# Kernel optimization log

Measured on AMD Instinct MI355X. Metric: run time of the kernel, lower is better.

The kernel has to match this reference:

```python
import jax, jax.numpy as jnp
import numpy as np

B, N, D = 8, 1024, 1024

def setup_inputs() -> dict:
    key = jax.random.key(0)
    k1, k2, k3, k4, k5 = jax.random.split(key, 5)
    x = jax.random.normal(k1, (B, N, D), dtype=jnp.float32)
    y = jax.random.normal(k2, (B, N, D), dtype=jnp.float32)
    adj = jax.random.uniform(k3, (B, N, N), dtype=jnp.float32)
    adj_sumrow = jnp.sum(adj, axis=-1, keepdims=True)  # [B, N, 1], row-sum normalizer
    W = jax.random.normal(k4, (D, D), dtype=jnp.float32) * (1.0 / np.sqrt(D))
    b = jax.random.normal(k5, (D,), dtype=jnp.float32) * 0.02
    return {"x": x, "y": y, "adj": adj, "adj_sumrow": adj_sumrow, "W": W, "b": b}

def reference(x, y, adj, adj_sumrow, W, b):
    # GraphConvolutionCustom: project neighbor features, aggregate via dense adj,
    # normalize by row-sum, add bias and residual input x; then ReLU.
    # Dropout is identity in eval mode (training=False).
    support = jnp.einsum('bnd,de->bne', y, W)          # [B, N, D]
    agg = jnp.matmul(adj, support) / adj_sumrow        # [B, N, D]
    out = jax.nn.relu(agg + b + x)
    return out
```

## Files before the change

### kernel.cpp

```cpp
#include <hip/hip_runtime.h>
#include <hip/hip_bf16.h>
#include <stdint.h>


typedef float  f32x4  __attribute__((ext_vector_type(4)));
typedef __bf16 bf16x8 __attribute__((ext_vector_type(8)));

__device__ __forceinline__ unsigned short f2bf(float f) {
  union { float f; unsigned int u; } c; c.f = f;
  unsigned int u = c.u;
  u += 0x7FFFu + ((u >> 16) & 1u);
  return (unsigned short)(u >> 16);
}

__device__ __forceinline__ void async_cp16(const void* g, void* l) {
  __builtin_amdgcn_global_load_lds(
      (const __attribute__((address_space(1))) unsigned int*)g,
      (__attribute__((address_space(3))) unsigned int*)l, 16, 0, 0);
}

__device__ __forceinline__ void bar() { asm volatile("s_barrier" ::: "memory"); }


__global__ __launch_bounds__(256) void k_prep(
    const float4* __restrict__ y4, const float4* __restrict__ a4,
    ushort4* __restrict__ yb, ushort4* __restrict__ ab,
    const float* __restrict__ W, unsigned short* __restrict__ Wt)
{
  __shared__ float t[64][65];
  const int bid = blockIdx.x;
  if (bid < 16384) {
    const int i = bid * 256 + threadIdx.x;
    const bool isY = i < 2097152;
    const float4 v = isY ? y4[i] : a4[i - 2097152];
    ushort4 p;
    p.x = f2bf(v.x); p.y = f2bf(v.y); p.z = f2bf(v.z); p.w = f2bf(v.w);
    if (isY) yb[i] = p; else ab[i - 2097152] = p;
  } else {
    const int id = bid - 16384;
    const int n0 = (id & 15) * 64, k0 = (id >> 4) * 64;
    const int tx = threadIdx.x & 63, ty = threadIdx.x >> 6;
#pragma unroll
    for (int r = ty; r < 64; r += 4)
      t[r][tx] = W[(size_t)(k0 + r) * 1024 + n0 + tx];
    __syncthreads();
#pragma unroll
    for (int r = ty; r < 64; r += 4)
      Wt[(size_t)(n0 + r) * 1024 + k0 + tx] = f2bf(t[tx][r]);
  }
}


__device__ __forceinline__ void stage64(
    const unsigned short* __restrict__ A,  int sA,
    const unsigned short* __restrict__ Bt, int sB,
    int m0, int n0, int k0,
    unsigned short* la, unsigned short* lb,
    int wave, int rg, int colo)
{
#pragma unroll
  for (int s = 0; s < 4; ++s) {
    const int t = wave * 4 + s;
    async_cp16(A  + (size_t)(m0 + t * 8 + rg) * sA + k0 + colo, la + t * 512);
    async_cp16(Bt + (size_t)(n0 + t * 8 + rg) * sB + k0 + colo, lb + t * 512);
  }
}

__device__ __forceinline__ void compute64(
    const unsigned short* la, const unsigned short* lb,
    f32x4 acc[4][4], int wm, int wn, int quad, int l16)
{
#pragma unroll
  for (int h = 0; h < 2; ++h) {
    bf16x8 af[4], bfr[4];
#pragma unroll
    for (int i = 0; i < 4; ++i) {
      const int r = wm + i * 16 + l16;
      af[i] = *(const bf16x8*)(la + r * 64 + ((h * 4 + quad + r) & 7) * 8);
    }
#pragma unroll
    for (int j = 0; j < 4; ++j) {
      const int r = wn + j * 16 + l16;
      bfr[j] = *(const bf16x8*)(lb + r * 64 + ((h * 4 + quad + r) & 7) * 8);
    }
#pragma unroll
    for (int i = 0; i < 4; ++i)
#pragma unroll
      for (int j = 0; j < 4; ++j)
        acc[i][j] = __builtin_amdgcn_mfma_f32_16x16x32_bf16(af[i], bfr[j], acc[i][j], 0, 0, 0);
  }
}

__device__ __forceinline__ void gemm_dbuf(
    const unsigned short* __restrict__ A,  int sA,
    const unsigned short* __restrict__ Bt, int sB,
    int m0, int n0, f32x4 acc[4][4], unsigned short* lsm, int tid)
{
  const int lane = tid & 63, wave = tid >> 6;
  const int wm = (wave >> 1) * 64, wn = (wave & 1) * 64;
  const int quad = lane >> 4, l16 = lane & 15;
  const int rg = lane >> 3;
  const int colo = (((lane & 7) - rg) & 7) * 8;
  unsigned short* la0 = lsm;
  unsigned short* lb0 = lsm + 8192;
  unsigned short* la1 = lsm + 16384;
  unsigned short* lb1 = lsm + 24576;

  stage64(A, sA, Bt, sB, m0, n0, 0, la0, lb0, wave, rg, colo);
#pragma unroll 1
  for (int k0 = 0; k0 < 1024; k0 += 128) {
    stage64(A, sA, Bt, sB, m0, n0, k0 + 64, la1, lb1, wave, rg, colo);
    asm volatile("s_waitcnt vmcnt(8)" ::: "memory");
    bar();
    compute64(la0, lb0, acc, wm, wn, quad, l16);
    bar();
    if (k0 + 128 < 1024) {
      stage64(A, sA, Bt, sB, m0, n0, k0 + 128, la0, lb0, wave, rg, colo);
      asm volatile("s_waitcnt vmcnt(8)" ::: "memory");
    } else {
      asm volatile("s_waitcnt vmcnt(0)" ::: "memory");
    }
    bar();
    compute64(la1, lb1, acc, wm, wn, quad, l16);
    bar();
  }
}

__device__ __forceinline__ void zero_acc(f32x4 acc[4][4]) {
#pragma unroll
  for (int i = 0; i < 4; ++i)
#pragma unroll
    for (int j = 0; j < 4; ++j)
#pragma unroll
      for (int r = 0; r < 4; ++r) acc[i][j][r] = 0.0f;
}


__global__ __launch_bounds__(256) void k_gemm1(
    const unsigned short* __restrict__ Wt,
    const unsigned short* __restrict__ Ybf,
    unsigned short* __restrict__ Sup2)
{
  __shared__ __align__(16) unsigned short lsm[4 * 8192];
  const int tid = threadIdx.x;
  const int n0 = blockIdx.x * 128, m0 = blockIdx.y * 128;

  f32x4 acc[4][4];
  zero_acc(acc);
  gemm_dbuf(Wt, 1024, Ybf, 1024, m0, n0, acc, lsm, tid);

  const int lane = tid & 63, wave = tid >> 6;
  const int wm = (wave >> 1) * 64, wn = (wave & 1) * 64;
  const int quad = lane >> 4, l16 = lane & 15;
#pragma unroll
  for (int i = 0; i < 4; ++i) {
    const int mb = m0 + wm + i * 16 + quad * 4;
#pragma unroll
    for (int r = 0; r < 4; ++r) {
      unsigned short* row = Sup2 + ((size_t)(mb + r) << 13);
#pragma unroll
      for (int j = 0; j < 4; ++j)
        row[n0 + wn + j * 16 + l16] = f2bf(acc[i][j][r]);
    }
  }
}


__global__ __launch_bounds__(256) void k_gemm2(
    const unsigned short* __restrict__ AdjBf,
    const unsigned short* __restrict__ Sup2,
    const float* __restrict__ x,
    const float* __restrict__ sumrow,
    const float* __restrict__ bias,
    float* __restrict__ out)
{
  __shared__ __align__(16) unsigned short lsm[4 * 8192];
  const int tid = threadIdx.x;
  const int n0 = blockIdx.x * 128, m0 = blockIdx.y * 128, b = blockIdx.z;

  f32x4 acc[4][4];
  zero_acc(acc);
  gemm_dbuf(AdjBf + ((size_t)b << 20), 1024,
            Sup2 + ((size_t)b << 10), 8192,
            m0, n0, acc, lsm, tid);

  const float* xb = x   + ((size_t)b << 20);
  float*       ob = out + ((size_t)b << 20);
  const float* sr = sumrow + ((size_t)b << 10);
  const int lane = tid & 63, wave = tid >> 6;
  const int wm = (wave >> 1) * 64, wn = (wave & 1) * 64;
  const int quad = lane >> 4, l16 = lane & 15;

  float bv[4];
#pragma unroll
  for (int j = 0; j < 4; ++j) bv[j] = bias[n0 + wn + j * 16 + l16];

#pragma unroll
  for (int i = 0; i < 4; ++i) {
    const int mb = m0 + wm + i * 16 + quad * 4;
#pragma unroll
    for (int r = 0; r < 4; ++r) {
      const int m = mb + r;
      const float inv = 1.0f / sr[m];
#pragma unroll
      for (int j = 0; j < 4; ++j) {
        const int n = n0 + wn + j * 16 + l16;
        const size_t idx = (((size_t)m) << 10) + n;
        float v = acc[i][j][r] * inv + bv[j] + xb[idx];
        ob[idx] = fmaxf(v, 0.0f);
      }
    }
  }
}


extern "C" void kernel_launch(void* const* d_in, const int* in_sizes, int n_in,
                              void* d_out, int out_size, void* d_ws, size_t ws_size,
                              hipStream_t stream) {
  const float* x      = (const float*)d_in[0];
  const float* y      = (const float*)d_in[1];
  const float* adj    = (const float*)d_in[2];
  const float* sumrow = (const float*)d_in[3];
  const float* W      = (const float*)d_in[4];
  const float* bias   = (const float*)d_in[5];
  float* out = (float*)d_out;

  char* ws = (char*)d_ws;
  unsigned short* ybf   = (unsigned short*)(ws);
  unsigned short* adjbf = (unsigned short*)(ws + ((size_t)16 << 20));
  unsigned short* wt    = (unsigned short*)(ws + ((size_t)32 << 20));
  unsigned short* sup2  = (unsigned short*)(ws + ((size_t)34 << 20));

  k_prep<<<dim3(16640), dim3(256), 0, stream>>>(
      (const float4*)y, (const float4*)adj, (ushort4*)ybf, (ushort4*)adjbf, W, wt);
  k_gemm1<<<dim3(64, 8), dim3(256), 0, stream>>>(wt, ybf, sup2);
  k_gemm2<<<dim3(8, 8, 8), dim3(256), 0, stream>>>(adjbf, sup2, x, sumrow, bias, out);
}
```

Baseline: 196.7 us.

## Shrink GEMM tiles to 128x64 with K-step 32 for higher occupancy

Both GEMM kernels move from 128x128 output tiles with a 64-wide K stage to 128x64 tiles with a 32-wide K stage. The LDS swizzle changes to fit the 4-chunk rows, launch bounds request 4 blocks per SM, and the grids double. The aim is to fill more CUs, since the old grids had only 512 blocks, and to hide latency through occupancy. The cost is lower arithmetic intensity per tile, more global and LDS traffic, and twice as many barriers per K.

```diff
diff --git a/kernel.cpp b/kernel.cpp
--- a/kernel.cpp
+++ b/kernel.cpp
@@ -20,6 +20,8 @@
 }
 
 __device__ __forceinline__ void bar() { asm volatile("s_barrier" ::: "memory"); }
+
+__device__ __forceinline__ int swz(int c, int r) { return (c + r + (r >> 1)) & 3; }
 
 
 __global__ __launch_bounds__(256) void k_prep(
@@ -51,106 +53,111 @@
 }
 
 
-__device__ __forceinline__ void stage64(
+__device__ __forceinline__ void stage32(
     const unsigned short* __restrict__ A,  int sA,
     const unsigned short* __restrict__ Bt, int sB,
     int m0, int n0, int k0,
     unsigned short* la, unsigned short* lb,
-    int wave, int rg, int colo)
-{
-#pragma unroll
-  for (int s = 0; s < 4; ++s) {
-    const int t = wave * 4 + s;
-    async_cp16(A  + (size_t)(m0 + t * 8 + rg) * sA + k0 + colo, la + t * 512);
-    async_cp16(Bt + (size_t)(n0 + t * 8 + rg) * sB + k0 + colo, lb + t * 512);
-  }
-}
-
-__device__ __forceinline__ void compute64(
+    int wave, int lane)
+{
+  const int p = lane & 3;
+#pragma unroll
+  for (int s = 0; s < 2; ++s) {
+    const int gid = wave * 128 + s * 64 + lane;
+    const int r = gid >> 2;
+    const int c = (p - r - (r >> 1)) & 3;
+    async_cp16(A + (size_t)(m0 + r) * sA + k0 + c * 8,
+               la + (wave * 128 + s * 64) * 8);
+  }
+  {
+    const int gid = wave * 64 + lane;
+    const int r = gid >> 2;
+    const int c = (p - r - (r >> 1)) & 3;
+    async_cp16(Bt + (size_t)(n0 + r) * sB + k0 + c * 8,
+               lb + (wave * 64) * 8);
+  }
+}
+
+__device__ __forceinline__ void compute32(
     const unsigned short* la, const unsigned short* lb,
-    f32x4 acc[4][4], int wm, int wn, int quad, int l16)
-{
-#pragma unroll
-  for (int h = 0; h < 2; ++h) {
-    bf16x8 af[4], bfr[4];
-#pragma unroll
-    for (int i = 0; i < 4; ++i) {
-      const int r = wm + i * 16 + l16;
-      af[i] = *(const bf16x8*)(la + r * 64 + ((h * 4 + quad + r) & 7) * 8);
-    }
-#pragma unroll
-    for (int j = 0; j < 4; ++j) {
-      const int r = wn + j * 16 + l16;
-      bfr[j] = *(const bf16x8*)(lb + r * 64 + ((h * 4 + quad + r) & 7) * 8);
-    }
-#pragma unroll
-    for (int i = 0; i < 4; ++i)
-#pragma unroll
-      for (int j = 0; j < 4; ++j)
-        acc[i][j] = __builtin_amdgcn_mfma_f32_16x16x32_bf16(af[i], bfr[j], acc[i][j], 0, 0, 0);
-  }
-}
-
-__device__ __forceinline__ void gemm_dbuf(
+    f32x4 acc[4][2], int wm, int wn, int quad, int l16)
+{
+  bf16x8 af[4], bfr[2];
+#pragma unroll
+  for (int i = 0; i < 4; ++i) {
+    const int r = wm + i * 16 + l16;
+    af[i] = *(const bf16x8*)(la + r * 32 + swz(quad, r) * 8);
+  }
+#pragma unroll
+  for (int j = 0; j < 2; ++j) {
+    const int r = wn + j * 16 + l16;
+    bfr[j] = *(const bf16x8*)(lb + r * 32 + swz(quad, r) * 8);
+  }
+#pragma unroll
+  for (int i = 0; i < 4; ++i)
+#pragma unroll
+    for (int j = 0; j < 2; ++j)
+      acc[i][j] = __builtin_amdgcn_mfma_f32_16x16x32_bf16(af[i], bfr[j], acc[i][j], 0, 0, 0);
+}
+
+__device__ __forceinline__ void gemm_dbuf32(
     const unsigned short* __restrict__ A,  int sA,
     const unsigned short* __restrict__ Bt, int sB,
-    int m0, int n0, f32x4 acc[4][4], unsigned short* lsm, int tid)
+    int m0, int n0, f32x4 acc[4][2], unsigned short* lsm, int tid)
 {
   const int lane = tid & 63, wave = tid >> 6;
-  const int wm = (wave >> 1) * 64, wn = (wave & 1) * 64;
+  const int wm = (wave >> 1) * 64, wn = (wave & 1) * 32;
   const int quad = lane >> 4, l16 = lane & 15;
-  const int rg = lane >> 3;
-  const int colo = (((lane & 7) - rg) & 7) * 8;
   unsigned short* la0 = lsm;
-  unsigned short* lb0 = lsm + 8192;
-  unsigned short* la1 = lsm + 16384;
-  unsigned short* lb1 = lsm + 24576;
-
-  stage64(A, sA, Bt, sB, m0, n0, 0, la0, lb0, wave, rg, colo);
+  unsigned short* lb0 = lsm + 4096;
+  unsigned short* la1 = lsm + 6144;
+  unsigned short* lb1 = lsm + 10240;
+
+  stage32(A, sA, Bt, sB, m0, n0, 0, la0, lb0, wave, lane);
 #pragma unroll 1
-  for (int k0 = 0; k0 < 1024; k0 += 128) {
-    stage64(A, sA, Bt, sB, m0, n0, k0 + 64, la1, lb1, wave, rg, colo);
-    asm volatile("s_waitcnt vmcnt(8)" ::: "memory");
-    bar();
-    compute64(la0, lb0, acc, wm, wn, quad, l16);
-    bar();
-    if (k0 + 128 < 1024) {
-      stage64(A, sA, Bt, sB, m0, n0, k0 + 128, la0, lb0, wave, rg, colo);
-      asm volatile("s_waitcnt vmcnt(8)" ::: "memory");
+  for (int k0 = 0; k0 < 1024; k0 += 64) {
+    stage32(A, sA, Bt, sB, m0, n0, k0 + 32, la1, lb1, wave, lane);
+    asm volatile("s_waitcnt vmcnt(3)" ::: "memory");
+    bar();
+    compute32(la0, lb0, acc, wm, wn, quad, l16);
+    bar();
+    if (k0 + 64 < 1024) {
+      stage32(A, sA, Bt, sB, m0, n0, k0 + 64, la0, lb0, wave, lane);
+      asm volatile("s_waitcnt vmcnt(3)" ::: "memory");
     } else {
       asm volatile("s_waitcnt vmcnt(0)" ::: "memory");
     }
     bar();
-    compute64(la1, lb1, acc, wm, wn, quad, l16);
-    bar();
-  }
-}
-
-__device__ __forceinline__ void zero_acc(f32x4 acc[4][4]) {
+    compute32(la1, lb1, acc, wm, wn, quad, l16);
+    bar();
+  }
+}
+
+__device__ __forceinline__ void zero_acc(f32x4 acc[4][2]) {
 #pragma unroll
   for (int i = 0; i < 4; ++i)
 #pragma unroll
-    for (int j = 0; j < 4; ++j)
+    for (int j = 0; j < 2; ++j)
 #pragma unroll
       for (int r = 0; r < 4; ++r) acc[i][j][r] = 0.0f;
 }
 
 
-__global__ __launch_bounds__(256) void k_gemm1(
+__global__ __launch_bounds__(256, 4) void k_gemm1(
     const unsigned short* __restrict__ Wt,
     const unsigned short* __restrict__ Ybf,
     unsigned short* __restrict__ Sup2)
 {
-  __shared__ __align__(16) unsigned short lsm[4 * 8192];
+  __shared__ __align__(16) unsigned short lsm[12288];
   const int tid = threadIdx.x;
-  const int n0 = blockIdx.x * 128, m0 = blockIdx.y * 128;
-
-  f32x4 acc[4][4];
+  const int n0 = blockIdx.x * 64, m0 = blockIdx.y * 128;
+
+  f32x4 acc[4][2];
   zero_acc(acc);
-  gemm_dbuf(Wt, 1024, Ybf, 1024, m0, n0, acc, lsm, tid);
+  gemm_dbuf32(Wt, 1024, Ybf, 1024, m0, n0, acc, lsm, tid);
 
   const int lane = tid & 63, wave = tid >> 6;
-  const int wm = (wave >> 1) * 64, wn = (wave & 1) * 64;
+  const int wm = (wave >> 1) * 64, wn = (wave & 1) * 32;
   const int quad = lane >> 4, l16 = lane & 15;
 #pragma unroll
   for (int i = 0; i < 4; ++i) {
@@ -159,14 +166,14 @@
     for (int r = 0; r < 4; ++r) {
       unsigned short* row = Sup2 + ((size_t)(mb + r) << 13);
 #pragma unroll
-      for (int j = 0; j < 4; ++j)
+      for (int j = 0; j < 2; ++j)
         row[n0 + wn + j * 16 + l16] = f2bf(acc[i][j][r]);
     }
   }
 }
 
 
-__global__ __launch_bounds__(256) void k_gemm2(
+__global__ __launch_bounds__(256, 4) void k_gemm2(
     const unsigned short* __restrict__ AdjBf,
     const unsigned short* __restrict__ Sup2,
     const float* __restrict__ x,
@@ -174,26 +181,26 @@
     const float* __restrict__ bias,
     float* __restrict__ out)
 {
-  __shared__ __align__(16) unsigned short lsm[4 * 8192];
+  __shared__ __align__(16) unsigned short lsm[12288];
   const int tid = threadIdx.x;
-  const int n0 = blockIdx.x * 128, m0 = blockIdx.y * 128, b = blockIdx.z;
-
-  f32x4 acc[4][4];
+  const int n0 = blockIdx.x * 64, m0 = blockIdx.y * 128, b = blockIdx.z;
+
+  f32x4 acc[4][2];
   zero_acc(acc);
-  gemm_dbuf(AdjBf + ((size_t)b << 20), 1024,
-            Sup2 + ((size_t)b << 10), 8192,
-            m0, n0, acc, lsm, tid);
+  gemm_dbuf32(AdjBf + ((size_t)b << 20), 1024,
+              Sup2 + ((size_t)b << 10), 8192,
+              m0, n0, acc, lsm, tid);
 
   const float* xb = x   + ((size_t)b << 20);
   float*       ob = out + ((size_t)b << 20);
   const float* sr = sumrow + ((size_t)b << 10);
   const int lane = tid & 63, wave = tid >> 6;
-  const int wm = (wave >> 1) * 64, wn = (wave & 1) * 64;
+  const int wm = (wave >> 1) * 64, wn = (wave & 1) * 32;
   const int quad = lane >> 4, l16 = lane & 15;
 
-  float bv[4];
-#pragma unroll
-  for (int j = 0; j < 4; ++j) bv[j] = bias[n0 + wn + j * 16 + l16];
+  float bv[2];
+#pragma unroll
+  for (int j = 0; j < 2; ++j) bv[j] = bias[n0 + wn + j * 16 + l16];
 
 #pragma unroll
   for (int i = 0; i < 4; ++i) {
@@ -203,7 +210,7 @@
       const int m = mb + r;
       const float inv = 1.0f / sr[m];
 #pragma unroll
-      for (int j = 0; j < 4; ++j) {
+      for (int j = 0; j < 2; ++j) {
         const int n = n0 + wn + j * 16 + l16;
         const size_t idx = (((size_t)m) << 10) + n;
         float v = acc[i][j][r] * inv + bv[j] + xb[idx];
@@ -233,6 +240,6 @@
 
   k_prep<<<dim3(16640), dim3(256), 0, stream>>>(
       (const float4*)y, (const float4*)adj, (ushort4*)ybf, (ushort4*)adjbf, W, wt);
-  k_gemm1<<<dim3(64, 8), dim3(256), 0, stream>>>(wt, ybf, sup2);
-  k_gemm2<<<dim3(8, 8, 8), dim3(256), 0, stream>>>(adjbf, sup2, x, sumrow, bias, out);
-}
+  k_gemm1<<<dim3(128, 8), dim3(256), 0, stream>>>(wt, ybf, sup2);
+  k_gemm2<<<dim3(16, 8, 8), dim3(256), 0, stream>>>(adjbf, sup2, x, sumrow, bias, out);
+}
```

Result: slower. 217.6 us (+10.6%).

## Fuse fp32-to-bf16 conversion of y and adj into GEMM tile loads

Applied to the files above, without the earlier changes.

Drops the separate prep pass that converted y and adj to bf16 in workspace. Each GEMM now loads fp32 tiles into registers, converts and packs them to bf16, and writes them to LDS, while the other operand still streams in asynchronously. Blocks grow to 512 threads with 256x128 tiles, and block indices are remapped for XCD and batch locality. This removes a full read-write round trip of the large tensors, but the register-staged path adds register pressure and conversion ALU work inside the main loop.

```diff
diff --git a/kernel.cpp b/kernel.cpp
--- a/kernel.cpp
+++ b/kernel.cpp
@@ -6,11 +6,11 @@
 typedef float  f32x4  __attribute__((ext_vector_type(4)));
 typedef __bf16 bf16x8 __attribute__((ext_vector_type(8)));
 
-__device__ __forceinline__ unsigned short f2bf(float f) {
+__device__ __forceinline__ unsigned int f2bf(float f) {
   union { float f; unsigned int u; } c; c.f = f;
   unsigned int u = c.u;
   u += 0x7FFFu + ((u >> 16) & 1u);
-  return (unsigned short)(u >> 16);
+  return u >> 16;
 }
 
 __device__ __forceinline__ void async_cp16(const void* g, void* l) {
@@ -20,53 +20,28 @@
 }
 
 __device__ __forceinline__ void bar() { asm volatile("s_barrier" ::: "memory"); }
-
-
-__global__ __launch_bounds__(256) void k_prep(
-    const float4* __restrict__ y4, const float4* __restrict__ a4,
-    ushort4* __restrict__ yb, ushort4* __restrict__ ab,
+#define VMCNT0()  asm volatile("s_waitcnt vmcnt(0)" ::: "memory")
+#define LGKM0()   asm volatile("s_waitcnt lgkmcnt(0)" ::: "memory")
+
+
+__global__ __launch_bounds__(256) void k_prep_w(
     const float* __restrict__ W, unsigned short* __restrict__ Wt)
 {
   __shared__ float t[64][65];
-  const int bid = blockIdx.x;
-  if (bid < 16384) {
-    const int i = bid * 256 + threadIdx.x;
-    const bool isY = i < 2097152;
-    const float4 v = isY ? y4[i] : a4[i - 2097152];
-    ushort4 p;
-    p.x = f2bf(v.x); p.y = f2bf(v.y); p.z = f2bf(v.z); p.w = f2bf(v.w);
-    if (isY) yb[i] = p; else ab[i - 2097152] = p;
-  } else {
-    const int id = bid - 16384;
-    const int n0 = (id & 15) * 64, k0 = (id >> 4) * 64;
-    const int tx = threadIdx.x & 63, ty = threadIdx.x >> 6;
-#pragma unroll
-    for (int r = ty; r < 64; r += 4)
-      t[r][tx] = W[(size_t)(k0 + r) * 1024 + n0 + tx];
-    __syncthreads();
-#pragma unroll
-    for (int r = ty; r < 64; r += 4)
-      Wt[(size_t)(n0 + r) * 1024 + k0 + tx] = f2bf(t[tx][r]);
-  }
-}
-
-
-__device__ __forceinline__ void stage64(
-    const unsigned short* __restrict__ A,  int sA,
-    const unsigned short* __restrict__ Bt, int sB,
-    int m0, int n0, int k0,
-    unsigned short* la, unsigned short* lb,
-    int wave, int rg, int colo)
-{
-#pragma unroll
-  for (int s = 0; s < 4; ++s) {
-    const int t = wave * 4 + s;
-    async_cp16(A  + (size_t)(m0 + t * 8 + rg) * sA + k0 + colo, la + t * 512);
-    async_cp16(Bt + (size_t)(n0 + t * 8 + rg) * sB + k0 + colo, lb + t * 512);
-  }
-}
-
-__device__ __forceinline__ void compute64(
+  const int id = blockIdx.x;
+  const int n0 = (id & 15) * 64, k0 = (id >> 4) * 64;
+  const int tx = threadIdx.x & 63, ty = threadIdx.x >> 6;
+#pragma unroll
+  for (int r = ty; r < 64; r += 4)
+    t[r][tx] = W[(size_t)(k0 + r) * 1024 + n0 + tx];
+  __syncthreads();
+#pragma unroll
+  for (int r = ty; r < 64; r += 4)
+    Wt[(size_t)(n0 + r) * 1024 + k0 + tx] = (unsigned short)f2bf(t[tx][r]);
+}
+
+
+__device__ __forceinline__ void compute_tile(
     const unsigned short* la, const unsigned short* lb,
     f32x4 acc[4][4], int wm, int wn, int quad, int l16)
 {
@@ -83,130 +58,220 @@
       const int r = wn + j * 16 + l16;
       bfr[j] = *(const bf16x8*)(lb + r * 64 + ((h * 4 + quad + r) & 7) * 8);
     }
+    __builtin_amdgcn_s_setprio(1);
 #pragma unroll
     for (int i = 0; i < 4; ++i)
 #pragma unroll
       for (int j = 0; j < 4; ++j)
-        acc[i][j] = __builtin_amdgcn_mfma_f32_16x16x32_bf16(af[i], bfr[j], acc[i][j], 0, 0, 0);
-  }
-}
-
-__device__ __forceinline__ void gemm_dbuf(
-    const unsigned short* __restrict__ A,  int sA,
-    const unsigned short* __restrict__ Bt, int sB,
-    int m0, int n0, f32x4 acc[4][4], unsigned short* lsm, int tid)
+        acc[i][j] = __builtin_amdgcn_mfma_f32_16x16x32_bf16(
+            af[i], bfr[j], acc[i][j], 0, 0, 0);
+    __builtin_amdgcn_s_setprio(0);
+  }
+}
+
+__device__ __forceinline__ void zero_acc(f32x4 acc[4][4]) {
+#pragma unroll
+  for (int i = 0; i < 4; ++i)
+#pragma unroll
+    for (int j = 0; j < 4; ++j)
+#pragma unroll
+      for (int r = 0; r < 4; ++r) acc[i][j][r] = 0.0f;
+}
+
+
+__global__ __launch_bounds__(512, 2) void k_gemm1(
+    const unsigned short* __restrict__ Wt,
+    const float* __restrict__ Y,
+    unsigned short* __restrict__ Sup2)
 {
+  __shared__ __align__(16) unsigned short lsm[2 * 24576];
+  const int tid = threadIdx.x;
+  const int xcd = blockIdx.x & 7, slot = blockIdx.x >> 3;
+  const int m0 = (slot >> 3) * 256;
+  const int n0 = (xcd * 8 + (slot & 7)) * 128;
+
   const int lane = tid & 63, wave = tid >> 6;
   const int wm = (wave >> 1) * 64, wn = (wave & 1) * 64;
   const int quad = lane >> 4, l16 = lane & 15;
   const int rg = lane >> 3;
   const int colo = (((lane & 7) - rg) & 7) * 8;
-  unsigned short* la0 = lsm;
-  unsigned short* lb0 = lsm + 8192;
-  unsigned short* la1 = lsm + 16384;
-  unsigned short* lb1 = lsm + 24576;
-
-  stage64(A, sA, Bt, sB, m0, n0, 0, la0, lb0, wave, rg, colo);
-#pragma unroll 1
-  for (int k0 = 0; k0 < 1024; k0 += 128) {
-    stage64(A, sA, Bt, sB, m0, n0, k0 + 64, la1, lb1, wave, rg, colo);
-    asm volatile("s_waitcnt vmcnt(8)" ::: "memory");
-    bar();
-    compute64(la0, lb0, acc, wm, wn, quad, l16);
-    bar();
-    if (k0 + 128 < 1024) {
-      stage64(A, sA, Bt, sB, m0, n0, k0 + 128, la0, lb0, wave, rg, colo);
-      asm volatile("s_waitcnt vmcnt(8)" ::: "memory");
-    } else {
-      asm volatile("s_waitcnt vmcnt(0)" ::: "memory");
-    }
-    bar();
-    compute64(la1, lb1, acc, wm, wn, quad, l16);
-    bar();
-  }
-}
-
-__device__ __forceinline__ void zero_acc(f32x4 acc[4][4]) {
-#pragma unroll
-  for (int i = 0; i < 4; ++i)
-#pragma unroll
-    for (int j = 0; j < 4; ++j)
-#pragma unroll
-      for (int r = 0; r < 4; ++r) acc[i][j][r] = 0.0f;
-}
-
-
-__global__ __launch_bounds__(256) void k_gemm1(
-    const unsigned short* __restrict__ Wt,
-    const unsigned short* __restrict__ Ybf,
-    unsigned short* __restrict__ Sup2)
-{
-  __shared__ __align__(16) unsigned short lsm[4 * 8192];
-  const int tid = threadIdx.x;
-  const int n0 = blockIdx.x * 128, m0 = blockIdx.y * 128;
+
+  const int r0 = tid >> 3;
+  const int cb = tid & 7;
+  const int pb = (cb + r0) & 7;
 
   f32x4 acc[4][4];
   zero_acc(acc);
-  gemm_dbuf(Wt, 1024, Ybf, 1024, m0, n0, acc, lsm, tid);
-
-  const int lane = tid & 63, wave = tid >> 6;
-  const int wm = (wave >> 1) * 64, wn = (wave & 1) * 64;
-  const int quad = lane >> 4, l16 = lane & 15;
-#pragma unroll
-  for (int i = 0; i < 4; ++i) {
-    const int mb = m0 + wm + i * 16 + quad * 4;
+
+  float4 br[2][2];
+
+  auto stageA = [&](int k0, unsigned short* la) {
+#pragma unroll
+    for (int s = 0; s < 4; ++s) {
+      const int row0 = (wave * 4 + s) * 8;
+      async_cp16(Wt + (size_t)(m0 + row0 + rg) * 1024 + k0 + colo, la + row0 * 64);
+    }
+  };
+  auto loadB = [&](int k0) {
+#pragma unroll
+    for (int s = 0; s < 2; ++s) {
+      const float* p = Y + (size_t)(n0 + r0 + 64 * s) * 1024 + k0 + cb * 8;
+      br[s][0] = *(const float4*)p;
+      br[s][1] = *(const float4*)(p + 4);
+    }
+  };
+  auto writeB = [&](unsigned short* lb) {
+#pragma unroll
+    for (int s = 0; s < 2; ++s) {
+      uint4 pk;
+      pk.x = f2bf(br[s][0].x) | (f2bf(br[s][0].y) << 16);
+      pk.y = f2bf(br[s][0].z) | (f2bf(br[s][0].w) << 16);
+      pk.z = f2bf(br[s][1].x) | (f2bf(br[s][1].y) << 16);
+      pk.w = f2bf(br[s][1].z) | (f2bf(br[s][1].w) << 16);
+      *(uint4*)(lb + (r0 + 64 * s) * 64 + pb * 8) = pk;
+    }
+  };
+
+  unsigned short* buf0 = lsm;
+  unsigned short* buf1 = lsm + 24576;
+
+  stageA(0, buf0);
+  loadB(0);
+  writeB(buf0 + 16384);
+  VMCNT0(); LGKM0();
+  __builtin_amdgcn_sched_barrier(0);
+  bar();
+
+#pragma unroll 1
+  for (int T = 0; T < 16; ++T) {
+    unsigned short* cb_ = (T & 1) ? buf1 : buf0;
+    unsigned short* nb_ = (T & 1) ? buf0 : buf1;
+    if (T < 15) { stageA((T + 1) * 64, nb_); loadB((T + 1) * 64); }
+    compute_tile(cb_, cb_ + 16384, acc, wm, wn, quad, l16);
+    if (T < 15) {
+      writeB(nb_ + 16384);
+      VMCNT0(); LGKM0();
+      __builtin_amdgcn_sched_barrier(0);
+      bar();
+    }
+  }
+
+#pragma unroll
+  for (int mi = 0; mi < 4; ++mi) {
+    const int mb = m0 + wm + mi * 16 + quad * 4;
 #pragma unroll
     for (int r = 0; r < 4; ++r) {
       unsigned short* row = Sup2 + ((size_t)(mb + r) << 13);
 #pragma unroll
-      for (int j = 0; j < 4; ++j)
-        row[n0 + wn + j * 16 + l16] = f2bf(acc[i][j][r]);
-    }
-  }
-}
-
-
-__global__ __launch_bounds__(256) void k_gemm2(
-    const unsigned short* __restrict__ AdjBf,
+      for (int nj = 0; nj < 4; ++nj)
+        row[n0 + wn + nj * 16 + l16] = (unsigned short)f2bf(acc[mi][nj][r]);
+    }
+  }
+}
+
+
+__global__ __launch_bounds__(512, 2) void k_gemm2(
+    const float* __restrict__ Adj,
     const unsigned short* __restrict__ Sup2,
     const float* __restrict__ x,
     const float* __restrict__ sumrow,
     const float* __restrict__ bias,
     float* __restrict__ out)
 {
-  __shared__ __align__(16) unsigned short lsm[4 * 8192];
+  __shared__ __align__(16) unsigned short lsm[2 * 24576];
   const int tid = threadIdx.x;
-  const int n0 = blockIdx.x * 128, m0 = blockIdx.y * 128, b = blockIdx.z;
+  const int b = blockIdx.x & 7, slot = blockIdx.x >> 3;
+  const int m0 = (slot >> 3) * 256, n0 = (slot & 7) * 128;
+
+  const float* Ab = Adj + ((size_t)b << 20);
+  const unsigned short* Bt = Sup2 + ((size_t)b << 10);
+
+  const int lane = tid & 63, wave = tid >> 6;
+  const int wm = (wave >> 1) * 64, wn = (wave & 1) * 64;
+  const int quad = lane >> 4, l16 = lane & 15;
+  const int rg = lane >> 3;
+  const int colo = (((lane & 7) - rg) & 7) * 8;
+
+  const int r0 = tid >> 3;
+  const int ca = tid & 7;
+  const int pa = (ca + r0) & 7;
 
   f32x4 acc[4][4];
   zero_acc(acc);
-  gemm_dbuf(AdjBf + ((size_t)b << 20), 1024,
-            Sup2 + ((size_t)b << 10), 8192,
-            m0, n0, acc, lsm, tid);
+
+  float4 ar[4][2];
+
+  auto loadA = [&](int k0) {
+#pragma unroll
+    for (int s = 0; s < 4; ++s) {
+      const float* p = Ab + (size_t)(m0 + r0 + 64 * s) * 1024 + k0 + ca * 8;
+      ar[s][0] = *(const float4*)p;
+      ar[s][1] = *(const float4*)(p + 4);
+    }
+  };
+  auto writeA = [&](unsigned short* la) {
+#pragma unroll
+    for (int s = 0; s < 4; ++s) {
+      uint4 pk;
+      pk.x = f2bf(ar[s][0].x) | (f2bf(ar[s][0].y) << 16);
+      pk.y = f2bf(ar[s][0].z) | (f2bf(ar[s][0].w) << 16);
+      pk.z = f2bf(ar[s][1].x) | (f2bf(ar[s][1].y) << 16);
+      pk.w = f2bf(ar[s][1].z) | (f2bf(ar[s][1].w) << 16);
+      *(uint4*)(la + (r0 + 64 * s) * 64 + pa * 8) = pk;
+    }
+  };
+  auto stageB = [&](int k0, unsigned short* lb) {
+#pragma unroll
+    for (int s = 0; s < 2; ++s) {
+      const int row0 = (wave * 2 + s) * 8;
+      async_cp16(Bt + (size_t)(n0 + row0 + rg) * 8192 + k0 + colo, lb + row0 * 64);
+    }
+  };
+
+  unsigned short* buf0 = lsm;
+  unsigned short* buf1 = lsm + 24576;
+
+  loadA(0);
+  stageB(0, buf0 + 16384);
+  writeA(buf0);
+  VMCNT0(); LGKM0();
+  __builtin_amdgcn_sched_barrier(0);
+  bar();
+
+#pragma unroll 1
+  for (int T = 0; T < 16; ++T) {
+    unsigned short* cb_ = (T & 1) ? buf1 : buf0;
+    unsigned short* nb_ = (T & 1) ? buf0 : buf1;
+    if (T < 15) { loadA((T + 1) * 64); stageB((T + 1) * 64, nb_ + 16384); }
+    compute_tile(cb_, cb_ + 16384, acc, wm, wn, quad, l16);
+    if (T < 15) {
+      writeA(nb_);
+      VMCNT0(); LGKM0();
+      __builtin_amdgcn_sched_barrier(0);
+      bar();
+    }
+  }
 
   const float* xb = x   + ((size_t)b << 20);
   float*       ob = out + ((size_t)b << 20);
   const float* sr = sumrow + ((size_t)b << 10);
-  const int lane = tid & 63, wave = tid >> 6;
-  const int wm = (wave >> 1) * 64, wn = (wave & 1) * 64;
-  const int quad = lane >> 4, l16 = lane & 15;
 
   float bv[4];
 #pragma unroll
-  for (int j = 0; j < 4; ++j) bv[j] = bias[n0 + wn + j * 16 + l16];
-
-#pragma unroll
-  for (int i = 0; i < 4; ++i) {
-    const int mb = m0 + wm + i * 16 + quad * 4;
+  for (int nj = 0; nj < 4; ++nj) bv[nj] = bias[n0 + wn + nj * 16 + l16];
+
+#pragma unroll
+  for (int mi = 0; mi < 4; ++mi) {
+    const int mb = m0 + wm + mi * 16 + quad * 4;
 #pragma unroll
     for (int r = 0; r < 4; ++r) {
       const int m = mb + r;
       const float inv = 1.0f / sr[m];
 #pragma unroll
-      for (int j = 0; j < 4; ++j) {
-        const int n = n0 + wn + j * 16 + l16;
+      for (int nj = 0; nj < 4; ++nj) {
+        const int n = n0 + wn + nj * 16 + l16;
         const size_t idx = (((size_t)m) << 10) + n;
-        float v = acc[i][j][r] * inv + bv[j] + xb[idx];
+        float v = acc[mi][nj][r] * inv + bv[nj] + xb[idx];
         ob[idx] = fmaxf(v, 0.0f);
       }
     }
@@ -226,13 +291,10 @@
   float* out = (float*)d_out;
 
   char* ws = (char*)d_ws;
-  unsigned short* ybf   = (unsigned short*)(ws);
-  unsigned short* adjbf = (unsigned short*)(ws + ((size_t)16 << 20));
-  unsigned short* wt    = (unsigned short*)(ws + ((size_t)32 << 20));
-  unsigned short* sup2  = (unsigned short*)(ws + ((size_t)34 << 20));
-
-  k_prep<<<dim3(16640), dim3(256), 0, stream>>>(
-      (const float4*)y, (const float4*)adj, (ushort4*)ybf, (ushort4*)adjbf, W, wt);
-  k_gemm1<<<dim3(64, 8), dim3(256), 0, stream>>>(wt, ybf, sup2);
-  k_gemm2<<<dim3(8, 8, 8), dim3(256), 0, stream>>>(adjbf, sup2, x, sumrow, bias, out);
-}
+  unsigned short* wt   = (unsigned short*)(ws);
+  unsigned short* sup2 = (unsigned short*)(ws + ((size_t)2 << 20));
+
+  k_prep_w<<<dim3(256), dim3(256), 0, stream>>>(W, wt);
+  k_gemm1<<<dim3(256), dim3(512), 0, stream>>>(wt, y, sup2);
+  k_gemm2<<<dim3(256), dim3(512), 0, stream>>>(adj, sup2, x, sumrow, bias, out);
+}
```

After: 219.6 us. 11.7% more time.
